# Performance work log

Measured on AMD Instinct MI355X. Metric: run time of the kernel, lower is better.

The kernel has to match this reference:

```python
import jax, jax.numpy as jnp
import numpy as np

ALPHA = 0.2
USE_SEMI_HARD = True
EPS = 1e-12

B, K, D, N_NEG = 16, 16, 256, 16384


def setup_inputs() -> dict:
    key = jax.random.key(0)
    k1, k2, k3, k4, k5 = jax.random.split(key, 5)
    Z1t = jax.random.normal(k1, (B, K, D), dtype=jnp.float32)
    Z2t = jax.random.normal(k2, (B, K, D), dtype=jnp.float32)
    matching = jax.random.randint(k3, (B, K), 0, K)
    negatives_pool = jax.random.normal(k4, (N_NEG, D), dtype=jnp.float32)
    # Build SPD shared covariance: R R^T / d + I
    R = jax.random.normal(k5, (B, D, D), dtype=jnp.float32)
    Sigma_plus = jnp.einsum('bde,bfe->bdf', R, R) / D + jnp.eye(D, dtype=jnp.float32)
    return {"Z1t": Z1t, "Z2t": Z2t, "matching": matching,
            "negatives_pool": negatives_pool, "Sigma_plus": Sigma_plus}


def reference(Z1t, Z2t, matching, negatives_pool, Sigma_plus):
    # A = Sigma^{-1}, one inverse per batch element (replaces per-pair solves)
    A = jnp.linalg.inv(Sigma_plus)                                   # [B,d,d]

    # positive pairs: q = Z2t[b, matching[b,k]]
    q = jnp.take_along_axis(Z2t, matching[..., None], axis=1)        # [B,K,d]
    diff = Z1t - q                                                   # [B,K,d]
    d_pos = jnp.sqrt(jnp.clip(
        jnp.einsum('bkd,bde,bke->bk', diff, A, diff), EPS))          # [B,K]

    # all pairwise Mahalanobis distances p vs negatives via quadratic expansion:
    # ||p-n||_A^2 = p'Ap - 2 p'An + n'An
    PA = jnp.einsum('bkd,bde->bke', Z1t, A)                          # [B,K,d]
    pAp = jnp.sum(PA * Z1t, axis=-1)                                 # [B,K]
    pAn = jnp.einsum('bke,ne->bkn', PA, negatives_pool)              # [B,K,N]
    NA = jnp.einsum('ne,bef->bnf', negatives_pool, A)                # [B,N,d]
    nAn = jnp.sum(NA * negatives_pool[None], axis=-1)                # [B,N]
    d2 = pAp[..., None] - 2.0 * pAn + nAn[:, None, :]                # [B,K,N]
    d_negs = jnp.sqrt(jnp.clip(d2, EPS))                             # [B,K,N]

    min_all = jnp.min(d_negs, axis=-1)                               # [B,K]
    if USE_SEMI_HARD:
        # semi-hard: min over negatives farther than the positive
        masked = jnp.where(d_negs > d_pos[..., None], d_negs, jnp.inf)
        min_valid = jnp.min(masked, axis=-1)
        d_neg = jnp.where(jnp.isfinite(min_valid), min_valid, min_all)
    else:
        d_neg = min_all

    loss = jnp.mean(jnp.maximum(d_pos - d_neg + ALPHA, 0.0))
    return loss
```

## Files before the change

### kernel.cpp

```cpp
#include <hip/hip_runtime.h>
#include <hip/hip_bf16.h>

#define ALPHA_ 0.2f
#define EPS_ 1e-12f

typedef short short8 __attribute__((ext_vector_type(8)));
typedef unsigned short ushort4v __attribute__((ext_vector_type(4)));
typedef float f32x4 __attribute__((ext_vector_type(4)));

constexpr int BB = 16, KK = 16, DD = 256, NNEG = 16384;

constexpr size_t OFF_AF_H  = 1048576;
constexpr size_t OFF_XA_H  = 1048576;
constexpr size_t OFF_AF_L  = 1572864;
constexpr size_t OFF_XA_L  = 1572864;
constexpr size_t OFF_XB_H  = 2097152;
constexpr size_t OFF_XB_L  = 2621440;
constexpr size_t OFF_NH    = 3145728;
constexpr size_t OFF_T_H   = 3145728;
constexpr size_t OFF_C01   = 3149824;
constexpr size_t OFF_T_L   = 3670016;
constexpr size_t OFF_S_H   = 4194304;
constexpr size_t OFF_S_L   = 4718592;
constexpr size_t OFF_PA_H  = 5242880;
constexpr size_t OFF_PA_L  = 5275648;
constexpr size_t OFF_PAP   = 5308416;
constexpr size_t OFF_DPOS2 = 5308672;
constexpr size_t OFF_MINA  = 5308928;
constexpr size_t OFF_MINV  = 5309184;

__device__ inline unsigned short bf_hi(float x) {
    unsigned u = __float_as_uint(x);
    return (unsigned short)((u + 0x7fffu + ((u >> 16) & 1u)) >> 16);
}
__device__ inline float bf_tof(unsigned short h) { return __uint_as_float(((unsigned)h) << 16); }
__device__ inline void split2(float x, unsigned short& h, unsigned short& l) {
    h = bf_hi(x); l = bf_hi(x - bf_tof(h));
}

__global__ __launch_bounds__(256) void kbound(const float* __restrict__ Sig, float* __restrict__ c01) {
    int b = blockIdx.x, t = threadIdx.x;
    const float* S = Sig + (size_t)b * 65536;
    __shared__ float v[256];
    __shared__ float red[256];
    float cs = 0.f;
    for (int i = 0; i < 256; ++i) cs += fabsf(S[(size_t)i * 256 + t]);
    red[t] = cs; __syncthreads();
    for (int s = 128; s > 0; s >>= 1) { if (t < s) red[t] = fmaxf(red[t], red[t + s]); __syncthreads(); }
    float G = red[0]; __syncthreads();
    v[t] = 1.f; __syncthreads();
    for (int it = 0; it < 12; ++it) {
        float wv = 0.f;
        for (int i = 0; i < 256; ++i) wv = fmaf(S[(size_t)i * 256 + t], v[i], wv);
        red[t] = wv * wv; __syncthreads();
        for (int s = 128; s > 0; s >>= 1) { if (t < s) red[t] += red[t + s]; __syncthreads(); }
        float nrm = sqrtf(red[0]); __syncthreads();
        v[t] = wv / nrm; __syncthreads();
    }
    float w2 = 0.f;
    for (int i = 0; i < 256; ++i) w2 = fmaf(S[(size_t)i * 256 + t], v[i], w2);
    red[t] = w2 * v[t]; __syncthreads();
    for (int s = 128; s > 0; s >>= 1) { if (t < s) red[t] += red[t + s]; __syncthreads(); }
    if (t == 0) {
        float lam = red[0];
        float Bb = fminf(G, 1.06f * lam + 0.05f);
        float c1 = -2.f / (Bb + (Bb + 1.f) * (Bb + 1.f) * 0.25f);
        c01[b] = -c1 * (Bb + 1.f); c01[16 + b] = c1;
    }
}

__global__ __launch_bounds__(256) void kinit(const float* __restrict__ Sig, float* __restrict__ ws,
                                             const float* __restrict__ c01) {
    int idx = blockIdx.x * 256 + threadIdx.x;
    int b = idx >> 16, rc = idx & 65535;
    int r = rc >> 8, c = rc & 255;
    float v = Sig[idx];
    unsigned short h, l;
    split2(v, h, l);
    ((unsigned short*)(ws + OFF_S_H))[idx] = h; ((unsigned short*)(ws + OFF_S_L))[idx] = l;
    float x0 = c01[16 + b] * v + ((r == c) ? c01[b] : 0.f);
    split2(x0, h, l);
    ((unsigned short*)(ws + OFF_XA_H))[idx] = h; ((unsigned short*)(ws + OFF_XA_L))[idx] = l;
}

__global__ __launch_bounds__(256) void kmm(const unsigned short* __restrict__ PAh,
                                           const unsigned short* __restrict__ PAl,
                                           const unsigned short* __restrict__ PBh,
                                           const unsigned short* __restrict__ PBl,
                                           unsigned short* __restrict__ POh,
                                           unsigned short* __restrict__ POl, int pmode,
                                           const unsigned short* __restrict__ Rh,
                                           const unsigned short* __restrict__ Rl,
                                           unsigned short* __restrict__ ROh,
                                           unsigned short* __restrict__ ROl) {
    __shared__ unsigned short pAh[32 * 256];
    __shared__ unsigned short pAl[32 * 256];
    __shared__ unsigned short pBh[32 * 256];
    __shared__ unsigned short pBl[32 * 256];

    int lin = blockIdx.x;
    int x = lin & 7, qq = lin >> 3;
    int isP = (qq < 128) ? 1 : 0;
    int q2 = isP ? qq : (qq - 128);
    int b = x * 2 + (q2 >> 6);
    int tile = q2 & 63;
    int i0 = (tile >> 3) * 32, j0 = (tile & 7) * 32;
    size_t base = (size_t)b * 65536;
    const unsigned short* Ah = isP ? PAh : Rh;
    const unsigned short* Al = isP ? PAl : Rl;
    const unsigned short* Bh = isP ? PBh : Rh;
    const unsigned short* Bl = isP ? PBl : Rl;
    unsigned short* Ch = isP ? POh : ROh;
    unsigned short* Cl = isP ? POl : ROl;

    int t = threadIdx.x;
    {
        int row = t >> 3, oc = t & 7, rsw = row & 7;
        const unsigned short* gah = Ah + base + (size_t)(i0 + row) * 256 + oc * 32;
        const unsigned short* gal = Al + base + (size_t)(i0 + row) * 256 + oc * 32;
        const unsigned short* gbh = Bh + base + (size_t)(j0 + row) * 256 + oc * 32;
        const unsigned short* gbl = Bl + base + (size_t)(j0 + row) * 256 + oc * 32;
        #pragma unroll
        for (int k = 0; k < 4; ++k) {
            int sb = (((oc * 4 + k) ^ rsw)) * 8;
            *reinterpret_cast<short8*>(pAh + row * 256 + sb) = *reinterpret_cast<const short8*>(gah + k * 8);
            *reinterpret_cast<short8*>(pAl + row * 256 + sb) = *reinterpret_cast<const short8*>(gal + k * 8);
            *reinterpret_cast<short8*>(pBh + row * 256 + sb) = *reinterpret_cast<const short8*>(gbh + k * 8);
            *reinterpret_cast<short8*>(pBl + row * 256 + sb) = *reinterpret_cast<const short8*>(gbl + k * 8);
        }
    }
    __syncthreads();

    int lane = t & 63, w = t >> 6;
    int wi = w & 1, wj = w >> 1;
    int l15 = lane & 15, lg = lane >> 4;
    int rs = l15 & 7;
    int ra = (wi * 16 + l15) * 256;
    int rb = (wj * 16 + l15) * 256;
    f32x4 acc0 = {}, acc1 = {};
    #pragma unroll
    for (int c = 0; c < 8; ++c) {
        int eb = ((c * 4 + lg) ^ rs) * 8;
        short8 a_h = *reinterpret_cast<const short8*>(pAh + ra + eb);
        short8 a_l = *reinterpret_cast<const short8*>(pAl + ra + eb);
        short8 b_h = *reinterpret_cast<const short8*>(pBh + rb + eb);
        short8 b_l = *reinterpret_cast<const short8*>(pBl + rb + eb);
        if (c & 1) {
            acc1 = __builtin_amdgcn_mfma_f32_16x16x32_bf16(a_h, b_h, acc1, 0, 0, 0);
            acc1 = __builtin_amdgcn_mfma_f32_16x16x32_bf16(a_h, b_l, acc1, 0, 0, 0);
            acc1 = __builtin_amdgcn_mfma_f32_16x16x32_bf16(a_l, b_h, acc1, 0, 0, 0);
        } else {
            acc0 = __builtin_amdgcn_mfma_f32_16x16x32_bf16(a_h, b_h, acc0, 0, 0, 0);
            acc0 = __builtin_amdgcn_mfma_f32_16x16x32_bf16(a_h, b_l, acc0, 0, 0, 0);
            acc0 = __builtin_amdgcn_mfma_f32_16x16x32_bf16(a_l, b_h, acc0, 0, 0, 0);
        }
    }
    #pragma unroll
    for (int r = 0; r < 4; ++r) {
        int row = i0 + wi * 16 + 4 * lg + r;
        int col = j0 + wj * 16 + l15;
        float v = acc0[r] + acc1[r];
        size_t off = base + (size_t)row * 256 + col;
        if (isP) {
            if (pmode == 2) v = ((row == col) ? 1.f : 0.f) - v;
            else            v += bf_tof(PAh[off]) + bf_tof(PAl[off]);
        }
        unsigned short h, l; split2(v, h, l);
        Ch[off] = h; Cl[off] = l;
    }
}

__global__ __launch_bounds__(256) void kpack(const unsigned short* __restrict__ XH,
                                             const unsigned short* __restrict__ XL,
                                             unsigned short* __restrict__ FH,
                                             unsigned short* __restrict__ FL) {
    int g = blockIdx.x * 256 + threadIdx.x;
    int b = g >> 13, rem = g & 8191;
    int row = rem >> 5, eb = rem & 31;
    size_t src = (size_t)b * 65536 + (size_t)row * 256 + eb * 8;
    size_t dst = (size_t)b * 65536 + (size_t)eb * 2048 + row * 8;
    *reinterpret_cast<short8*>(FH + dst) = *reinterpret_cast<const short8*>(XH + src);
    *reinterpret_cast<short8*>(FL + dst) = *reinterpret_cast<const short8*>(XL + src);
}

__global__ __launch_bounds__(256) void kaux(const float* __restrict__ negs,
                                            unsigned short* __restrict__ NH,
                                            unsigned* __restrict__ mina,
                                            unsigned* __restrict__ minv,
                                            const float* __restrict__ Z1,
                                            const float* __restrict__ Z2,
                                            const int* __restrict__ match,
                                            const unsigned short* __restrict__ AH,
                                            const unsigned short* __restrict__ AL,
                                            float* __restrict__ ws) {
    __shared__ float z[DD], df[DD];
    __shared__ float red[256];
    int blk = blockIdx.x, t = threadIdx.x;
    if (blk < 2048) {
        size_t i8 = ((size_t)blk * 256 + t) * 8;
        f32x4 v0 = *reinterpret_cast<const f32x4*>(negs + i8);
        f32x4 v1 = *reinterpret_cast<const f32x4*>(negs + i8 + 4);
        short8 h;
        #pragma unroll
        for (int j = 0; j < 4; ++j) {
            h[j] = (short)bf_hi(v0[j]);
            h[4 + j] = (short)bf_hi(v1[j]);
        }
        *reinterpret_cast<short8*>(NH + i8) = h;
        if (blk == 0) { mina[t] = 0x7f800000u; minv[t] = 0x7f800000u; }
        return;
    }
    int bk = blk - 2048; int b = bk >> 4; int k = bk & 15;
    const unsigned short* Ah = AH + (size_t)b * 65536;
    const unsigned short* Al = AL + (size_t)b * 65536;
    int m = match[bk];
    float zv = Z1[(size_t)bk * DD + t];
    float qv = Z2[((size_t)b * KK + m) * DD + t];
    z[t] = zv; df[t] = zv - qv;
    __syncthreads();
    float pa = 0.f, da = 0.f;
    for (int e = 0; e < DD; ++e) {
        float Ae = bf_tof(Ah[(size_t)e * 256 + t]) + bf_tof(Al[(size_t)e * 256 + t]);
        pa = fmaf(z[e], Ae, pa);
        da = fmaf(df[e], Ae, da);
    }
    unsigned short ph, pl; split2(pa, ph, pl);
    size_t pidx = (size_t)b * 4096 + (size_t)(t >> 3) * 128 + k * 8 + (t & 7);
    ((unsigned short*)(ws + OFF_PA_H))[pidx] = ph;
    ((unsigned short*)(ws + OFF_PA_L))[pidx] = pl;
    float dfv = df[t];
    red[t] = pa * zv; __syncthreads();
    for (int s = 128; s > 0; s >>= 1) { if (t < s) red[t] += red[t + s]; __syncthreads(); }
    float pAp = red[0]; __syncthreads();
    red[t] = da * dfv; __syncthreads();
    for (int s = 128; s > 0; s >>= 1) { if (t < s) red[t] += red[t + s]; __syncthreads(); }
    if (t == 0) {
        ws[OFF_PAP + bk]   = pAp;
        ws[OFF_DPOS2 + bk] = fmaxf(red[0], EPS_);
    }
}

__global__ __launch_bounds__(512) void k3(const unsigned short* __restrict__ AFH,
                                          const unsigned short* __restrict__ AFL,
                                          const unsigned short* __restrict__ PFH,
                                          const unsigned short* __restrict__ PFL,
                                          const unsigned short* __restrict__ NH,
                                          const float* __restrict__ pap,
                                          const float* __restrict__ dpos2,
                                          unsigned* __restrict__ mina,
                                          unsigned* __restrict__ minv) {
    __shared__ unsigned short Bh[128 * 256];
    __shared__ float ep[3328];

    int lin = blockIdx.x;
    int x  = lin & 7;
    int q  = lin >> 3;
    int b  = q >> 4;
    int n0 = (x * 16 + (q & 15)) * 128;
    int t = threadIdx.x, lane = t & 63, w = t >> 6;
    int l15 = lane & 15, lg = lane >> 4;
    const unsigned short* Nh = NH + (size_t)n0 * 256;

    {
        int row = t >> 2, q4 = t & 3, rsw = row & 7;
        const unsigned short* gh = Nh + (size_t)row * 256 + q4 * 64;
        #pragma unroll
        for (int k = 0; k < 8; ++k) {
            int sblk = (q4 * 8 + k) ^ rsw;
            *reinterpret_cast<short8*>(Bh + row * 256 + sblk * 8) =
                *reinterpret_cast<const short8*>(gh + k * 8);
        }
    }
    __syncthreads();

    const unsigned short* aFh = AFH + (size_t)b * 65536 + (size_t)lg * 2048 + (w * 32 + l15) * 8;
    const unsigned short* aFl = AFL + (size_t)b * 65536 + (size_t)lg * 2048 + (w * 32 + l15) * 8;
    const unsigned short* pFh = PFH + (size_t)b * 4096 + (size_t)lg * 128 + l15 * 8;
    const unsigned short* pFl = PFL + (size_t)b * 4096 + (size_t)lg * 128 + l15 * 8;

    f32x4 acc0[8] = {}, acc1[8] = {};
    f32x4 accp = {};
    int rs0 = l15 & 7;

    #pragma unroll
    for (int c = 0; c < 8; ++c) {
        short8 ah0 = *reinterpret_cast<const short8*>(aFh + c * 8192);
        short8 al0 = *reinterpret_cast<const short8*>(aFl + c * 8192);
        short8 ah1 = *reinterpret_cast<const short8*>(aFh + c * 8192 + 128);
        short8 al1 = *reinterpret_cast<const short8*>(aFl + c * 8192 + 128);
        short8 ph_ = *reinterpret_cast<const short8*>(pFh + c * 512);
        short8 pl_ = *reinterpret_cast<const short8*>(pFl + c * 512);
        #pragma unroll
        for (int j = 0; j < 8; ++j) {
            int ro = (j * 16 + l15) * 256 + (((c * 4 + lg) ^ rs0) * 8);
            short8 bh = *reinterpret_cast<const short8*>(Bh + ro);
            acc0[j] = __builtin_amdgcn_mfma_f32_16x16x32_bf16(ah0, bh, acc0[j], 0, 0, 0);
            acc0[j] = __builtin_amdgcn_mfma_f32_16x16x32_bf16(al0, bh, acc0[j], 0, 0, 0);
            acc1[j] = __builtin_amdgcn_mfma_f32_16x16x32_bf16(ah1, bh, acc1[j], 0, 0, 0);
            acc1[j] = __builtin_amdgcn_mfma_f32_16x16x32_bf16(al1, bh, acc1[j], 0, 0, 0);
            if (w == j) {
                accp = __builtin_amdgcn_mfma_f32_16x16x32_bf16(ph_, bh, accp, 0, 0, 0);
                accp = __builtin_amdgcn_mfma_f32_16x16x32_bf16(pl_, bh, accp, 0, 0, 0);
            }
        }
    }

    float* pAn_l = ep;
    float* nAnp  = ep + 2176;
    float* nAn_l = ep + 3200;
    float* reda  = ep + 2176;
    float* redv  = ep + 2688;

    #pragma unroll
    for (int r = 0; r < 4; ++r)
        pAn_l[(w * 16 + l15) * 17 + 4 * lg + r] = accp[r];

    int bb = w * 4 + (lg >> 1);
    int sub = (lg & 1) * 4;
    #pragma unroll
    for (int j = 0; j < 8; ++j) {
        int n = j * 16 + l15;
        float p = 0.f;
        {
            ushort4v wh0 = *reinterpret_cast<const ushort4v*>(Bh + n * 256 + ((bb    ) ^ rs0) * 8 + sub);
            ushort4v wh1 = *reinterpret_cast<const ushort4v*>(Bh + n * 256 + ((bb + 2) ^ rs0) * 8 + sub);
            #pragma unroll
            for (int r = 0; r < 4; ++r) {
                p = fmaf(acc0[j][r], bf_tof(wh0[r]), p);
                p = fmaf(acc1[j][r], bf_tof(wh1[r]), p);
            }
        }
        p += __shfl_xor(p, 16);
        p += __shfl_xor(p, 32);
        if (lane < 16) nAnp[w * 128 + n] = p;
    }
    __syncthreads();
    if (t < 128) {
        float s = 0.f;
        #pragma unroll
        for (int ww = 0; ww < 8; ++ww) s += nAnp[ww * 128 + t];
        nAn_l[t] = s;
    }
    __syncthreads();
    {
        int tx = t & 15, ty = t >> 4;
        float pApk = pap[b * 16 + tx];
        float dp2  = dpos2[b * 16 + tx];
        float mn_a = __uint_as_float(0x7f800000u), mn_v = mn_a;
        #pragma unroll
        for (int ii = 0; ii < 4; ++ii) {
            int n = ty * 4 + ii;
            float d2v = pApk - 2.f * pAn_l[n * 17 + tx] + nAn_l[n];
            float cc = fmaxf(d2v, EPS_);
            mn_a = fminf(mn_a, cc);
            if (cc > dp2) mn_v = fminf(mn_v, cc);
        }
        reda[ty * 16 + tx] = mn_a; redv[ty * 16 + tx] = mn_v;
    }
    __syncthreads();
    if (t < 16) {
        float ra = reda[t], rv = redv[t];
        #pragma unroll
        for (int y = 1; y < 32; ++y) {
            ra = fminf(ra, reda[y * 16 + t]);
            rv = fminf(rv, redv[y * 16 + t]);
        }
        atomicMin(&mina[b * 16 + t], __float_as_uint(ra));
        atomicMin(&minv[b * 16 + t], __float_as_uint(rv));
    }
}

__global__ __launch_bounds__(256) void k5(const float* __restrict__ dpos2,
                                          const unsigned* __restrict__ mina,
                                          const unsigned* __restrict__ minv,
                                          float* __restrict__ out) {
    int t = threadIdx.x;
    __shared__ float red[256];
    float dp = sqrtf(dpos2[t]);
    unsigned mv = minv[t], ma = mina[t];
    unsigned sel = (mv < 0x7f800000u) ? mv : ma;
    float dn = sqrtf(__uint_as_float(sel));
    red[t] = fmaxf(dp - dn + ALPHA_, 0.f);
    __syncthreads();
    for (int s = 128; s > 0; s >>= 1) { if (t < s) red[t] += red[t + s]; __syncthreads(); }
    if (t == 0) out[0] = red[0] * (1.f / 256.f);
}

extern "C" void kernel_launch(void* const* d_in, const int* in_sizes, int n_in,
                              void* d_out, int out_size, void* d_ws, size_t ws_size,
                              hipStream_t stream) {
    (void)in_sizes; (void)n_in; (void)out_size; (void)ws_size;
    const float* Z1   = (const float*)d_in[0];
    const float* Z2   = (const float*)d_in[1];
    const int*   mat  = (const int*)d_in[2];
    const float* negs = (const float*)d_in[3];
    const float* Sig  = (const float*)d_in[4];
    float* ws = (float*)d_ws;
    unsigned short* S_H  = (unsigned short*)(ws + OFF_S_H);
    unsigned short* S_L  = (unsigned short*)(ws + OFF_S_L);
    unsigned short* XA_H = (unsigned short*)(ws + OFF_XA_H);
    unsigned short* XA_L = (unsigned short*)(ws + OFF_XA_L);
    unsigned short* XB_H = (unsigned short*)(ws + OFF_XB_H);
    unsigned short* XB_L = (unsigned short*)(ws + OFF_XB_L);
    unsigned short* T_H  = (unsigned short*)(ws + OFF_T_H);
    unsigned short* T_L  = (unsigned short*)(ws + OFF_T_L);
    unsigned short* AF_H = (unsigned short*)(ws + OFF_AF_H);
    unsigned short* AF_L = (unsigned short*)(ws + OFF_AF_L);
    unsigned short* PA_H = (unsigned short*)(ws + OFF_PA_H);
    unsigned short* PA_L = (unsigned short*)(ws + OFF_PA_L);
    unsigned short* NH   = (unsigned short*)(ws + OFF_NH);
    unsigned* mina = (unsigned*)(ws + OFF_MINA);
    unsigned* minv = (unsigned*)(ws + OFF_MINV);
    float* out = (float*)d_out;

    kbound<<<BB, 256, 0, stream>>>(Sig, ws + OFF_C01);
    kinit<<<4096, 256, 0, stream>>>(Sig, ws, ws + OFF_C01);

    kmm<<<1024, 256, 0, stream>>>(S_H, S_L, XA_H, XA_L, T_H, T_L, 2, S_H, S_L, T_H, T_L);
    kmm<<<2048, 256, 0, stream>>>(XA_H, XA_L, T_H, T_L, XB_H, XB_L, 3, T_H, T_L, S_H, S_L);
    kmm<<<2048, 256, 0, stream>>>(XB_H, XB_L, S_H, S_L, XA_H, XA_L, 3, S_H, S_L, T_H, T_L);
    kmm<<<1024, 256, 0, stream>>>(XA_H, XA_L, T_H, T_L, XB_H, XB_L, 3, S_H, S_L, T_H, T_L);

    kpack<<<512, 256, 0, stream>>>(XB_H, XB_L, AF_H, AF_L);
    kaux<<<2048 + BB * KK, 256, 0, stream>>>(negs, NH, mina, minv,
                                             Z1, Z2, mat, XB_H, XB_L, ws);
    k3<<<BB * NNEG / 128, 512, 0, stream>>>(AF_H, AF_L, PA_H, PA_L, NH,
                                            ws + OFF_PAP, ws + OFF_DPOS2, mina, minv);
    k5<<<1, 256, 0, stream>>>(ws + OFF_DPOS2, mina, minv, out);
}
```

Before: 251.8 us.

## Fold kpack into kaux and split k3 across 16 waves of 1024 threads

After: 264.4 us. +5.0%, slower.

```diff
diff --git a/kernel.cpp b/kernel.cpp
--- a/kernel.cpp
+++ b/kernel.cpp
@@ -170,19 +170,6 @@
     }
 }
 
-__global__ __launch_bounds__(256) void kpack(const unsigned short* __restrict__ XH,
-                                             const unsigned short* __restrict__ XL,
-                                             unsigned short* __restrict__ FH,
-                                             unsigned short* __restrict__ FL) {
-    int g = blockIdx.x * 256 + threadIdx.x;
-    int b = g >> 13, rem = g & 8191;
-    int row = rem >> 5, eb = rem & 31;
-    size_t src = (size_t)b * 65536 + (size_t)row * 256 + eb * 8;
-    size_t dst = (size_t)b * 65536 + (size_t)eb * 2048 + row * 8;
-    *reinterpret_cast<short8*>(FH + dst) = *reinterpret_cast<const short8*>(XH + src);
-    *reinterpret_cast<short8*>(FL + dst) = *reinterpret_cast<const short8*>(XL + src);
-}
-
 __global__ __launch_bounds__(256) void kaux(const float* __restrict__ negs,
                                             unsigned short* __restrict__ NH,
                                             unsigned* __restrict__ mina,
@@ -192,6 +179,8 @@
                                             const int* __restrict__ match,
                                             const unsigned short* __restrict__ AH,
                                             const unsigned short* __restrict__ AL,
+                                            unsigned short* __restrict__ FH,
+                                            unsigned short* __restrict__ FL,
                                             float* __restrict__ ws) {
     __shared__ float z[DD], df[DD];
     __shared__ float red[256];
@@ -208,6 +197,16 @@
         }
         *reinterpret_cast<short8*>(NH + i8) = h;
         if (blk == 0) { mina[t] = 0x7f800000u; minv[t] = 0x7f800000u; }
+        return;
+    }
+    if (blk >= 2304) {
+        int g = (blk - 2304) * 256 + t;
+        int b = g >> 13, rem = g & 8191;
+        int row = rem >> 5, eb = rem & 31;
+        size_t src = (size_t)b * 65536 + (size_t)row * 256 + eb * 8;
+        size_t dst = (size_t)b * 65536 + (size_t)eb * 2048 + row * 8;
+        *reinterpret_cast<short8*>(FH + dst) = *reinterpret_cast<const short8*>(AH + src);
+        *reinterpret_cast<short8*>(FL + dst) = *reinterpret_cast<const short8*>(AL + src);
         return;
     }
     int bk = blk - 2048; int b = bk >> 4; int k = bk & 15;
@@ -240,17 +239,17 @@
     }
 }
 
-__global__ __launch_bounds__(512) void k3(const unsigned short* __restrict__ AFH,
-                                          const unsigned short* __restrict__ AFL,
-                                          const unsigned short* __restrict__ PFH,
-                                          const unsigned short* __restrict__ PFL,
-                                          const unsigned short* __restrict__ NH,
-                                          const float* __restrict__ pap,
-                                          const float* __restrict__ dpos2,
-                                          unsigned* __restrict__ mina,
-                                          unsigned* __restrict__ minv) {
+__global__ __launch_bounds__(1024) void k3(const unsigned short* __restrict__ AFH,
+                                           const unsigned short* __restrict__ AFL,
+                                           const unsigned short* __restrict__ PFH,
+                                           const unsigned short* __restrict__ PFL,
+                                           const unsigned short* __restrict__ NH,
+                                           const float* __restrict__ pap,
+                                           const float* __restrict__ dpos2,
+                                           unsigned* __restrict__ mina,
+                                           unsigned* __restrict__ minv) {
     __shared__ unsigned short Bh[128 * 256];
-    __shared__ float ep[3328];
+    __shared__ float ep[4352];
 
     int lin = blockIdx.x;
     int x  = lin & 7;
@@ -262,42 +261,41 @@
     const unsigned short* Nh = NH + (size_t)n0 * 256;
 
     {
-        int row = t >> 2, q4 = t & 3, rsw = row & 7;
-        const unsigned short* gh = Nh + (size_t)row * 256 + q4 * 64;
-        #pragma unroll
-        for (int k = 0; k < 8; ++k) {
-            int sblk = (q4 * 8 + k) ^ rsw;
+        int row = t >> 3, oct = t & 7, rsw = row & 7;
+        const unsigned short* gh = Nh + (size_t)row * 256 + oct * 32;
+        #pragma unroll
+        for (int k = 0; k < 4; ++k) {
+            int sblk = (oct * 4 + k) ^ rsw;
             *reinterpret_cast<short8*>(Bh + row * 256 + sblk * 8) =
                 *reinterpret_cast<const short8*>(gh + k * 8);
         }
     }
     __syncthreads();
 
-    const unsigned short* aFh = AFH + (size_t)b * 65536 + (size_t)lg * 2048 + (w * 32 + l15) * 8;
-    const unsigned short* aFl = AFL + (size_t)b * 65536 + (size_t)lg * 2048 + (w * 32 + l15) * 8;
+    const unsigned short* aFh = AFH + (size_t)b * 65536 + (size_t)lg * 2048 + (w * 16 + l15) * 8;
+    const unsigned short* aFl = AFL + (size_t)b * 65536 + (size_t)lg * 2048 + (w * 16 + l15) * 8;
     const unsigned short* pFh = PFH + (size_t)b * 4096 + (size_t)lg * 128 + l15 * 8;
     const unsigned short* pFl = PFL + (size_t)b * 4096 + (size_t)lg * 128 + l15 * 8;
 
-    f32x4 acc0[8] = {}, acc1[8] = {};
+    f32x4 acc[8] = {};
     f32x4 accp = {};
     int rs0 = l15 & 7;
 
     #pragma unroll
     for (int c = 0; c < 8; ++c) {
-        short8 ah0 = *reinterpret_cast<const short8*>(aFh + c * 8192);
-        short8 al0 = *reinterpret_cast<const short8*>(aFl + c * 8192);
-        short8 ah1 = *reinterpret_cast<const short8*>(aFh + c * 8192 + 128);
-        short8 al1 = *reinterpret_cast<const short8*>(aFl + c * 8192 + 128);
-        short8 ph_ = *reinterpret_cast<const short8*>(pFh + c * 512);
-        short8 pl_ = *reinterpret_cast<const short8*>(pFl + c * 512);
+        short8 ah = *reinterpret_cast<const short8*>(aFh + c * 8192);
+        short8 al = *reinterpret_cast<const short8*>(aFl + c * 8192);
+        short8 ph_ = {}, pl_ = {};
+        if (w < 8) {
+            ph_ = *reinterpret_cast<const short8*>(pFh + c * 512);
+            pl_ = *reinterpret_cast<const short8*>(pFl + c * 512);
+        }
         #pragma unroll
         for (int j = 0; j < 8; ++j) {
             int ro = (j * 16 + l15) * 256 + (((c * 4 + lg) ^ rs0) * 8);
             short8 bh = *reinterpret_cast<const short8*>(Bh + ro);
-            acc0[j] = __builtin_amdgcn_mfma_f32_16x16x32_bf16(ah0, bh, acc0[j], 0, 0, 0);
-            acc0[j] = __builtin_amdgcn_mfma_f32_16x16x32_bf16(al0, bh, acc0[j], 0, 0, 0);
-            acc1[j] = __builtin_amdgcn_mfma_f32_16x16x32_bf16(ah1, bh, acc1[j], 0, 0, 0);
-            acc1[j] = __builtin_amdgcn_mfma_f32_16x16x32_bf16(al1, bh, acc1[j], 0, 0, 0);
+            acc[j] = __builtin_amdgcn_mfma_f32_16x16x32_bf16(ah, bh, acc[j], 0, 0, 0);
+            acc[j] = __builtin_amdgcn_mfma_f32_16x16x32_bf16(al, bh, acc[j], 0, 0, 0);
             if (w == j) {
                 accp = __builtin_amdgcn_mfma_f32_16x16x32_bf16(ph_, bh, accp, 0, 0, 0);
                 accp = __builtin_amdgcn_mfma_f32_16x16x32_bf16(pl_, bh, accp, 0, 0, 0);
@@ -307,28 +305,26 @@
 
     float* pAn_l = ep;
     float* nAnp  = ep + 2176;
-    float* nAn_l = ep + 3200;
+    float* nAn_l = ep + 4224;
     float* reda  = ep + 2176;
     float* redv  = ep + 2688;
 
-    #pragma unroll
-    for (int r = 0; r < 4; ++r)
-        pAn_l[(w * 16 + l15) * 17 + 4 * lg + r] = accp[r];
-
-    int bb = w * 4 + (lg >> 1);
+    if (w < 8) {
+        #pragma unroll
+        for (int r = 0; r < 4; ++r)
+            pAn_l[(w * 16 + l15) * 17 + 4 * lg + r] = accp[r];
+    }
+    int bb = 2 * w + (lg >> 1);
     int sub = (lg & 1) * 4;
     #pragma unroll
     for (int j = 0; j < 8; ++j) {
         int n = j * 16 + l15;
         float p = 0.f;
         {
-            ushort4v wh0 = *reinterpret_cast<const ushort4v*>(Bh + n * 256 + ((bb    ) ^ rs0) * 8 + sub);
-            ushort4v wh1 = *reinterpret_cast<const ushort4v*>(Bh + n * 256 + ((bb + 2) ^ rs0) * 8 + sub);
+            ushort4v wh0 = *reinterpret_cast<const ushort4v*>(Bh + n * 256 + ((bb ^ rs0) * 8) + sub);
             #pragma unroll
-            for (int r = 0; r < 4; ++r) {
-                p = fmaf(acc0[j][r], bf_tof(wh0[r]), p);
-                p = fmaf(acc1[j][r], bf_tof(wh1[r]), p);
-            }
+            for (int r = 0; r < 4; ++r)
+                p = fmaf(acc[j][r], bf_tof(wh0[r]), p);
         }
         p += __shfl_xor(p, 16);
         p += __shfl_xor(p, 32);
@@ -338,11 +334,11 @@
     if (t < 128) {
         float s = 0.f;
         #pragma unroll
-        for (int ww = 0; ww < 8; ++ww) s += nAnp[ww * 128 + t];
+        for (int ww = 0; ww < 16; ++ww) s += nAnp[ww * 128 + t];
         nAn_l[t] = s;
     }
     __syncthreads();
-    {
+    if (t < 512) {
         int tx = t & 15, ty = t >> 4;
         float pApk = pap[b * 16 + tx];
         float dp2  = dpos2[b * 16 + tx];
@@ -421,10 +417,10 @@
     kmm<<<2048, 256, 0, stream>>>(XB_H, XB_L, S_H, S_L, XA_H, XA_L, 3, S_H, S_L, T_H, T_L);
     kmm<<<1024, 256, 0, stream>>>(XA_H, XA_L, T_H, T_L, XB_H, XB_L, 3, S_H, S_L, T_H, T_L);
 
-    kpack<<<512, 256, 0, stream>>>(XB_H, XB_L, AF_H, AF_L);
-    kaux<<<2048 + BB * KK, 256, 0, stream>>>(negs, NH, mina, minv,
-                                             Z1, Z2, mat, XB_H, XB_L, ws);
-    k3<<<BB * NNEG / 128, 512, 0, stream>>>(AF_H, AF_L, PA_H, PA_L, NH,
-                                            ws + OFF_PAP, ws + OFF_DPOS2, mina, minv);
+    kaux<<<2048 + BB * KK + 512, 256, 0, stream>>>(negs, NH, mina, minv,
+                                                   Z1, Z2, mat, XB_H, XB_L,
+                                                   AF_H, AF_L, ws);
+    k3<<<BB * NNEG / 128, 1024, 0, stream>>>(AF_H, AF_L, PA_H, PA_L, NH,
+                                             ws + OFF_PAP, ws + OFF_DPOS2, mina, minv);
     k5<<<1, 256, 0, stream>>>(ws + OFF_DPOS2, mina, minv, out);
 }
```
